# Performance work log

Measured on AMD Instinct MI355X. Metric: run time of the kernel, lower is better.

Reference implementation:

```python
import jax, jax.numpy as jnp
import numpy as np

WS = 7       # window_size
SHIFT = 3    # shift_size
NH = 4       # num_heads


def _layernorm(x, g, b, eps=1e-5):
    m = jnp.mean(x, axis=-1, keepdims=True)
    v = jnp.mean((x - m) ** 2, axis=-1, keepdims=True)
    return (x - m) * jax.lax.rsqrt(v + eps) * g + b


def _mha(x, wq, bq, wk, bk, wv, bv, wo, bo):
    # x: [n, s, c]; weights stored as [in, out]
    n, s, c = x.shape
    dk = c // NH
    q = (x @ wq + bq).reshape(n, s, NH, dk).transpose(0, 2, 1, 3)
    k = (x @ wk + bk).reshape(n, s, NH, dk).transpose(0, 2, 1, 3)
    v = (x @ wv + bv).reshape(n, s, NH, dk).transpose(0, 2, 1, 3)
    scores = jnp.einsum('nhqd,nhkd->nhqk', q, k) / jnp.sqrt(jnp.float32(dk))
    attn = jax.nn.softmax(scores, axis=-1)  # dropout is identity in eval
    out = jnp.einsum('nhqk,nhkd->nhqd', attn, v)
    out = out.transpose(0, 2, 1, 3).reshape(n, s, c)
    return out @ wo + bo


def _window_partition(x):
    B, H, W, C = x.shape
    x = x.reshape(B, H // WS, WS, W // WS, WS, C)
    x = x.transpose(0, 1, 3, 2, 4, 5)
    return x.reshape(-1, WS * WS, C)


def _window_reverse(wins, H, W):
    C = wins.shape[-1]
    B = wins.shape[0] // ((H // WS) * (W // WS))
    x = wins.reshape(B, H // WS, W // WS, WS, WS, C)
    x = x.transpose(0, 1, 3, 2, 4, 5)
    return x.reshape(B, H, W, C)


def setup_inputs() -> dict:
    key = jax.random.key(0)
    ks = jax.random.split(key, 16)
    C = 128
    def w(k, shape):
        return jax.random.normal(k, shape, dtype=jnp.float32) * 0.02
    return {
        'x':  jax.random.normal(ks[0], (4, 56, 56, C), dtype=jnp.float32),
        'wq': w(ks[1], (C, C)), 'bq': jnp.zeros((C,), jnp.float32),
        'wk': w(ks[2], (C, C)), 'bk': jnp.zeros((C,), jnp.float32),
        'wv': w(ks[3], (C, C)), 'bv': jnp.zeros((C,), jnp.float32),
        'wo': w(ks[4], (C, C)), 'bo': jnp.zeros((C,), jnp.float32),
        'w1': w(ks[5], (C, 4 * C)), 'b1': jnp.zeros((4 * C,), jnp.float32),
        'w2': w(ks[6], (4 * C, C)), 'b2': jnp.zeros((C,), jnp.float32),
        'g1': jnp.ones((C,), jnp.float32), 'be1': jnp.zeros((C,), jnp.float32),
        'g2': jnp.ones((C,), jnp.float32), 'be2': jnp.zeros((C,), jnp.float32),
    }


def reference(x, wq, bq, wk, bk, wv, bv, wo, bo, w1, b1, w2, b2, g1, be1, g2, be2):
    B, H, W, C = x.shape
    # cyclic shift
    xs = jnp.roll(x, shift=(-SHIFT, -SHIFT), axis=(1, 2)) if SHIFT > 0 else x
    # windowed attention (note: original code replaces x, no residual here)
    wins = _window_partition(xs)                         # [B*nW, 49, C]
    attn_wins = _mha(wins, wq, bq, wk, bk, wv, bv, wo, bo)
    xs = _window_reverse(attn_wins, H, W)
    x = jnp.roll(xs, shift=(SHIFT, SHIFT), axis=(1, 2)) if SHIFT > 0 else xs
    # global attention residual branch (flatten H*W tokens)
    xf = x.reshape(B, H * W, C)
    xf = xf + _mha(_layernorm(xf, g1, be1), wq, bq, wk, bk, wv, bv, wo, bo)
    # MLP residual branch
    h = jax.nn.gelu(_layernorm(xf, g2, be2) @ w1 + b1, approximate=False)
    xf = xf + (h @ w2 + b2)
    return xf.reshape(B, H, W, C)
```

## Files before the change

kernel.cpp:

```cpp
#include <hip/hip_runtime.h>
#include <hip/hip_bf16.h>
#include <math.h>

#define NH 4
#define DK 32
#define CC 128
#define HW 56
#define SHIFT 3
#define NTOK 12544
#define S_GLB 3136
#define VTW_STRIDE 12608
#define SCALE_L2E 0.25503488f

typedef unsigned short u16;
typedef short bf16x8 __attribute__((ext_vector_type(8)));
typedef unsigned short u16x8 __attribute__((ext_vector_type(8)));
typedef float f32x4 __attribute__((ext_vector_type(4)));

static __device__ __forceinline__ u16 f2bf(float f) {
  unsigned int b = __builtin_bit_cast(unsigned int, f);
  return (u16)((b + 0x7FFFu + ((b >> 16) & 1u)) >> 16);
}
static __device__ __forceinline__ unsigned pk2bf(float a, float b) {
  unsigned r;
  asm("v_cvt_pk_bf16_f32 %0, %1, %2" : "=v"(r) : "v"(a), "v"(b));
  return r;
}
static __device__ __forceinline__ float fexp2(float x) {
  float r;
  asm("v_exp_f32 %0, %1" : "=v"(r) : "v"(x));
  return r;
}

__global__ __launch_bounds__(256) void cvt_all_k(
    const float* __restrict__ w1, const float* __restrict__ w2,
    const float* __restrict__ wq, const float* __restrict__ wk,
    const float* __restrict__ wv, const float* __restrict__ wo,
    u16* __restrict__ w1t, u16* __restrict__ w2t,
    u16* __restrict__ wqkvt, u16* __restrict__ wot) {
  const int idx = blockIdx.x * 256 + threadIdx.x;
  if (idx < 65536) {
    const int c = idx >> 7, r = idx & 127;
    w1t[idx] = f2bf(w1[r * 512 + c]);
  } else if (idx < 131072) {
    const int o = idx - 65536;
    const int c = o / 512, r = o - c * 512;
    w2t[o] = f2bf(w2[r * 128 + c]);
  } else {
    const int o = idx - 131072;
    const int which = o >> 14, oo = o & 16383;
    const int c = oo >> 7, r = oo & 127;
    const float* src = (which == 0) ? wq : (which == 1) ? wk : (which == 2) ? wv : wo;
    u16* dst = (which < 3) ? (wqkvt + which * 16384) : wot;
    dst[oo] = f2bf(src[r * 128 + c]);
  }
}

__global__ __launch_bounds__(256) void win_gather_k(
    const float* __restrict__ x, u16* __restrict__ xg) {
  const int t = blockIdx.x * 2 + (threadIdx.x >> 7);
  const int c = threadIdx.x & 127;
  const int win = t / 49, tok = t % 49;
  const int b = win >> 6, wrem = win & 63;
  const int wi = wrem >> 3, wj = wrem & 7;
  const int i = tok / 7, j = tok % 7;
  int hh = wi * 7 + i + SHIFT; if (hh >= HW) hh -= HW;
  int ww = wj * 7 + j + SHIFT; if (ww >= HW) ww -= HW;
  xg[(size_t)t * CC + c] = f2bf(x[((size_t)(b * HW + hh) * HW + ww) * CC + c]);
}

template <int PATH>
__global__ __launch_bounds__(256) void qkv_gemm_k(
    const u16* __restrict__ xin, const u16* __restrict__ wqkvt,
    const float* __restrict__ bq, const float* __restrict__ bk,
    const float* __restrict__ bv,
    u16* __restrict__ qo, u16* __restrict__ ko, u16* __restrict__ vto) {
  __shared__ __align__(16) u16 xs[64][136];
  __shared__ __align__(16) u16 wt[64][136];
  const int tid = threadIdx.x;
  const int w = tid >> 6, lane = tid & 63;
  const int lo = lane & 15, hi = lane >> 4, hi4 = hi * 4;
  const int m0 = blockIdx.x * 64;
  const int widx = blockIdx.y >> 1;
  const int n0 = (blockIdx.y & 1) * 64;
  {
    const int r = tid >> 2, sg = tid & 3;
    const u16* sx = &xin[(size_t)(m0 + r) * CC + sg * 32];
    const u16* sw = &wqkvt[(size_t)widx * CC * CC + (size_t)(n0 + r) * CC + sg * 32];
#pragma unroll
    for (int j = 0; j < 4; ++j) {
      *reinterpret_cast<u16x8*>(&xs[r][sg * 32 + j * 8]) = *reinterpret_cast<const u16x8*>(&sx[j * 8]);
      *reinterpret_cast<u16x8*>(&wt[r][sg * 32 + j * 8]) = *reinterpret_cast<const u16x8*>(&sw[j * 8]);
    }
  }
  __syncthreads();
  if (widx < 2) {
    const float* bias = (widx == 0) ? bq : bk;
    u16* outp = (widx == 0) ? qo : ko;
    const float oscale = (widx == 0) ? SCALE_L2E : 1.0f;
    f32x4 acc[4];
#pragma unroll
    for (int st = 0; st < 4; ++st) {
      const float b_ = bias[n0 + st * 16 + lo];
      acc[st] = (f32x4){b_, b_, b_, b_};
    }
#pragma unroll
    for (int kk = 0; kk < 4; ++kk) {
      const bf16x8 af = *reinterpret_cast<const bf16x8*>(&xs[w * 16 + lo][kk * 32 + 8 * hi]);
#pragma unroll
      for (int st = 0; st < 4; ++st) {
        const bf16x8 bfr = *reinterpret_cast<const bf16x8*>(&wt[st * 16 + lo][kk * 32 + 8 * hi]);
        acc[st] = __builtin_amdgcn_mfma_f32_16x16x32_bf16(af, bfr, acc[st], 0, 0, 0);
      }
    }
#pragma unroll
    for (int r = 0; r < 4; ++r) {
      const int mm = m0 + w * 16 + hi4 + r;
      size_t rowbase, hstride;
      if (PATH == 0) {
        const int win = mm / 49, tok = mm - win * 49;
        rowbase = ((size_t)(win * 4) * 49 + tok) * DK;
        hstride = (size_t)49 * DK;
      } else {
        const int b = mm / S_GLB, s = mm - b * S_GLB;
        rowbase = ((size_t)(b * 4) * S_GLB + s) * DK;
        hstride = (size_t)S_GLB * DK;
      }
#pragma unroll
      for (int st = 0; st < 4; ++st) {
        const int c = n0 + st * 16 + lo, h = c >> 5, d = c & 31;
        outp[rowbase + (size_t)h * hstride + d] = f2bf(acc[st][r] * oscale);
      }
    }
  } else {
    f32x4 bias4;
#pragma unroll
    for (int r = 0; r < 4; ++r) bias4[r] = bv[n0 + w * 16 + hi4 + r];
    f32x4 acc[4];
#pragma unroll
    for (int st = 0; st < 4; ++st) acc[st] = bias4;
#pragma unroll
    for (int kk = 0; kk < 4; ++kk) {
      const bf16x8 af = *reinterpret_cast<const bf16x8*>(&wt[w * 16 + lo][kk * 32 + 8 * hi]);
#pragma unroll
      for (int st = 0; st < 4; ++st) {
        const bf16x8 bfr = *reinterpret_cast<const bf16x8*>(&xs[st * 16 + lo][kk * 32 + 8 * hi]);
        acc[st] = __builtin_amdgcn_mfma_f32_16x16x32_bf16(af, bfr, acc[st], 0, 0, 0);
      }
    }
#pragma unroll
    for (int st = 0; st < 4; ++st) {
      const int mm = m0 + st * 16 + lo;
#pragma unroll
      for (int r = 0; r < 4; ++r) {
        const int c = n0 + w * 16 + hi4 + r;
        if (PATH == 0) {
          vto[(size_t)c * VTW_STRIDE + mm] = f2bf(acc[st][r]);
        } else {
          const int b = mm / S_GLB, s = mm - b * S_GLB;
          vto[((size_t)b * CC + c) * S_GLB + s] = f2bf(acc[st][r]);
        }
      }
    }
  }
}

__global__ __launch_bounds__(256) void win_attn_k(
    const u16* __restrict__ qw, const u16* __restrict__ kw,
    const u16* __restrict__ vtw, u16* __restrict__ aow) {
  __shared__ __align__(16) u16 psh[4][16][72];
  const int tid = threadIdx.x;
  const int wvi = tid >> 6, lane = tid & 63;
  const int lo = lane & 15, hi = lane >> 4, hi4 = hi * 4;
  const int wh = blockIdx.x * 4 + wvi;
  const int win = wh >> 2, hd = wh & 3;
  const f32x4 zero4 = {0.f, 0.f, 0.f, 0.f};
  bf16x8 ones;
#pragma unroll
  for (int j = 0; j < 8; ++j) ones[j] = (short)0x3F80;

  bf16x8 kf[4], vf[2][2];
#pragma unroll
  for (int st = 0; st < 4; ++st)
    kf[st] = *reinterpret_cast<const bf16x8*>(&kw[((size_t)wh * 49 + st * 16 + lo) * DK + 8 * hi]);
#pragma unroll
  for (int dst = 0; dst < 2; ++dst)
#pragma unroll
    for (int kch = 0; kch < 2; ++kch)
      vf[dst][kch] = *reinterpret_cast<const bf16x8*>(
          &vtw[(size_t)(hd * DK + dst * 16 + lo) * VTW_STRIDE + win * 49 + kch * 32 + 8 * hi]);

#pragma unroll
  for (int g = 0; g < 4; ++g) {
    const bf16x8 qf = *reinterpret_cast<const bf16x8*>(
        &qw[((size_t)wh * 49 + g * 16 + lo) * DK + 8 * hi]);
    f32x4 s4[4];
#pragma unroll
    for (int st = 0; st < 4; ++st) {
      s4[st] = __builtin_amdgcn_mfma_f32_16x16x32_bf16(kf[st], qf, zero4, 0, 0, 0);
#pragma unroll
      for (int r = 0; r < 4; ++r)
        if (st * 16 + hi4 + r >= 49) s4[st][r] = -1e30f;
    }
#pragma unroll
    for (int st = 0; st < 4; ++st) {
      uint2 pk;
      pk.x = pk2bf(fexp2(s4[st][0]), fexp2(s4[st][1]));
      pk.y = pk2bf(fexp2(s4[st][2]), fexp2(s4[st][3]));
      *reinterpret_cast<uint2*>(&psh[wvi][lo][st * 16 + hi4]) = pk;
    }
    asm volatile("" ::: "memory");
    f32x4 acc0 = zero4, acc1 = zero4, lacc = zero4;
#pragma unroll
    for (int kch = 0; kch < 2; ++kch) {
      const bf16x8 pa = *reinterpret_cast<const bf16x8*>(&psh[wvi][lo][kch * 32 + 8 * hi]);
      acc0 = __builtin_amdgcn_mfma_f32_16x16x32_bf16(pa, vf[0][kch], acc0, 0, 0, 0);
      acc1 = __builtin_amdgcn_mfma_f32_16x16x32_bf16(pa, vf[1][kch], acc1, 0, 0, 0);
      lacc = __builtin_amdgcn_mfma_f32_16x16x32_bf16(pa, ones, lacc, 0, 0, 0);
    }
#pragma unroll
    for (int r = 0; r < 4; ++r) {
      const int qrow = g * 16 + hi4 + r;
      if (qrow < 49) {
        const float rl = 1.0f / lacc[r];
        const size_t tw = (size_t)win * 49 + qrow;
        aow[tw * CC + hd * DK + lo] = f2bf(acc0[r] * rl);
        aow[tw * CC + hd * DK + 16 + lo] = f2bf(acc1[r] * rl);
      }
    }
  }
}

__global__ __launch_bounds__(256) void glb_attn_k(
    const u16* __restrict__ qg, const u16* __restrict__ kg,
    const u16* __restrict__ vtg, u16* __restrict__ aog) {
  __shared__ __align__(16) u16 ksh[2][64][40];
  __shared__ __align__(16) u16 vtsh[2][32][72];
  __shared__ __align__(16) u16 psh[4][16][72];
  const int tid = threadIdx.x;
  const int w = tid >> 6, lane = tid & 63;
  const int lo = lane & 15, hi = lane >> 4, hi4 = hi * 4;
  const int bh = blockIdx.y;
  const int q0 = blockIdx.x * 64;
  const f32x4 zero4 = {0.f, 0.f, 0.f, 0.f};
  bf16x8 ones;
#pragma unroll
  for (int j = 0; j < 8; ++j) ones[j] = (short)0x3F80;

  const bf16x8 qfrag = *reinterpret_cast<const bf16x8*>(
      &qg[((size_t)bh * S_GLB + q0 + w * 16 + lo) * DK + 8 * hi]);
  const u16* kg0 = kg + (size_t)bh * S_GLB * DK;
  const u16* vg0 = vtg + (size_t)bh * DK * S_GLB;

  f32x4 oacc0 = zero4, oacc1 = zero4, lacc = zero4;

  const int krow = tid >> 2, kc = tid & 3;
  const int vrow = tid >> 3, vc = tid & 7;

  *reinterpret_cast<u16x8*>(&ksh[0][krow][kc * 8]) =
      *reinterpret_cast<const u16x8*>(&kg0[(size_t)krow * DK + kc * 8]);
  *reinterpret_cast<u16x8*>(&vtsh[0][vrow][vc * 8]) =
      *reinterpret_cast<const u16x8*>(&vg0[(size_t)vrow * S_GLB + vc * 8]);
  __syncthreads();

  for (int kt = 0; kt < 49; ++kt) {
    const int cur = kt & 1, nxt = cur ^ 1;
    u16x8 knext, vnext;
    const bool have = (kt + 1) < 49;
    if (have) {
      knext = *reinterpret_cast<const u16x8*>(
          &kg0[(size_t)((kt + 1) * 64 + krow) * DK + kc * 8]);
      vnext = *reinterpret_cast<const u16x8*>(
          &vg0[(size_t)vrow * S_GLB + (kt + 1) * 64 + vc * 8]);
    }
    f32x4 s4[4];
#pragma unroll
    for (int st = 0; st < 4; ++st) {
      const bf16x8 kfrag = *reinterpret_cast<const bf16x8*>(&ksh[cur][st * 16 + lo][8 * hi]);
      s4[st] = __builtin_amdgcn_mfma_f32_16x16x32_bf16(kfrag, qfrag, zero4, 0, 0, 0);
    }
#pragma unroll
    for (int st = 0; st < 4; ++st) {
      uint2 pk;
      pk.x = pk2bf(fexp2(s4[st][0]), fexp2(s4[st][1]));
      pk.y = pk2bf(fexp2(s4[st][2]), fexp2(s4[st][3]));
      *reinterpret_cast<uint2*>(&psh[w][lo][st * 16 + hi4]) = pk;
    }
    asm volatile("" ::: "memory");
#pragma unroll
    for (int kch = 0; kch < 2; ++kch) {
      const bf16x8 pa = *reinterpret_cast<const bf16x8*>(&psh[w][lo][kch * 32 + 8 * hi]);
      const bf16x8 v0 = *reinterpret_cast<const bf16x8*>(&vtsh[cur][lo][kch * 32 + 8 * hi]);
      const bf16x8 v1 = *reinterpret_cast<const bf16x8*>(&vtsh[cur][16 + lo][kch * 32 + 8 * hi]);
      oacc0 = __builtin_amdgcn_mfma_f32_16x16x32_bf16(pa, v0, oacc0, 0, 0, 0);
      oacc1 = __builtin_amdgcn_mfma_f32_16x16x32_bf16(pa, v1, oacc1, 0, 0, 0);
      lacc = __builtin_amdgcn_mfma_f32_16x16x32_bf16(pa, ones, lacc, 0, 0, 0);
    }
    if (have) {
      *reinterpret_cast<u16x8*>(&ksh[nxt][krow][kc * 8]) = knext;
      *reinterpret_cast<u16x8*>(&vtsh[nxt][vrow][vc * 8]) = vnext;
    }
    __syncthreads();
  }

  const int b = bh >> 2, hd = bh & 3;
#pragma unroll
  for (int r = 0; r < 4; ++r) {
    const float rl = 1.0f / lacc[r];
    const size_t t = (size_t)b * S_GLB + q0 + w * 16 + hi4 + r;
    aog[t * CC + hd * DK + lo] = f2bf(oacc0[r] * rl);
    aog[t * CC + hd * DK + 16 + lo] = f2bf(oacc1[r] * rl);
  }
}

template <int MODE>
__global__ __launch_bounds__(256) void proj_gemm_k(
    const u16* __restrict__ ain, const u16* __restrict__ wot,
    const float* __restrict__ bo, const float* __restrict__ resid,
    float* __restrict__ xfo) {
  __shared__ __align__(16) u16 xs[64][136];
  __shared__ __align__(16) u16 wt[64][136];
  const int tid = threadIdx.x;
  const int w = tid >> 6, lane = tid & 63;
  const int lo = lane & 15, hi = lane >> 4, hi4 = hi * 4;
  const int m0 = blockIdx.x * 64;
  const int n0 = blockIdx.y * 64;
  {
    const int r = tid >> 2, sg = tid & 3;
    const u16* sx = &ain[(size_t)(m0 + r) * CC + sg * 32];
    const u16* sw = &wot[(size_t)(n0 + r) * CC + sg * 32];
#pragma unroll
    for (int j = 0; j < 4; ++j) {
      *reinterpret_cast<u16x8*>(&xs[r][sg * 32 + j * 8]) = *reinterpret_cast<const u16x8*>(&sx[j * 8]);
      *reinterpret_cast<u16x8*>(&wt[r][sg * 32 + j * 8]) = *reinterpret_cast<const u16x8*>(&sw[j * 8]);
    }
  }
  __syncthreads();
  f32x4 acc[4];
#pragma unroll
  for (int st = 0; st < 4; ++st) {
    const float b_ = bo[n0 + st * 16 + lo];
    acc[st] = (f32x4){b_, b_, b_, b_};
  }
#pragma unroll
  for (int kk = 0; kk < 4; ++kk) {
    const bf16x8 af = *reinterpret_cast<const bf16x8*>(&xs[w * 16 + lo][kk * 32 + 8 * hi]);
#pragma unroll
    for (int st = 0; st < 4; ++st) {
      const bf16x8 bfr = *reinterpret_cast<const bf16x8*>(&wt[st * 16 + lo][kk * 32 + 8 * hi]);
      acc[st] = __builtin_amdgcn_mfma_f32_16x16x32_bf16(af, bfr, acc[st], 0, 0, 0);
    }
  }
#pragma unroll
  for (int r = 0; r < 4; ++r) {
    const int mm = m0 + w * 16 + hi4 + r;
    size_t trow;
    if (MODE == 0) {
      const int win = mm / 49, tok = mm - win * 49;
      const int b = win >> 6, wi = (win >> 3) & 7, wj = win & 7;
      const int ii = tok / 7, jj = tok - ii * 7;
      int hr = wi * 7 + ii + SHIFT; if (hr >= HW) hr -= HW;
      int wr = wj * 7 + jj + SHIFT; if (wr >= HW) wr -= HW;
      trow = ((size_t)b * S_GLB + hr * HW + wr) * CC;
    } else {
      trow = (size_t)mm * CC;
    }
#pragma unroll
    for (int st = 0; st < 4; ++st) {
      const int c = n0 + st * 16 + lo;
      if (MODE == 1)
        xfo[trow + c] = resid[trow + c] + acc[st][r];
      else
        xfo[trow + c] = acc[st][r];
    }
  }
}

__global__ __launch_bounds__(128) void ln_k(
    const float* __restrict__ xf, const float* __restrict__ g,
    const float* __restrict__ be, u16* __restrict__ ybf) {
  __shared__ float xs[8][CC];
  __shared__ float red[8][2];
  const int t0 = blockIdx.x * 8;
  const int tid = threadIdx.x;
  for (int t2 = 0; t2 < 8; ++t2) xs[t2][tid] = xf[(size_t)(t0 + t2) * CC + tid];
  __syncthreads();
  const int wvi = tid >> 6, lane = tid & 63;
  for (int t2 = wvi * 4; t2 < wvi * 4 + 4; ++t2) {
    const float v0 = xs[t2][lane], v1 = xs[t2][64 + lane];
    float s = v0 + v1, sq = v0 * v0 + v1 * v1;
#pragma unroll
    for (int off = 1; off < 64; off <<= 1) { s += __shfl_xor(s, off); sq += __shfl_xor(sq, off); }
    if (lane == 0) {
      const float mu = s * 0.0078125f;
      const float var = sq * 0.0078125f - mu * mu;
      red[t2][0] = mu; red[t2][1] = rsqrtf(var + 1e-5f);
    }
  }
  __syncthreads();
  const float gg = g[tid], bb = be[tid];
  for (int t2 = 0; t2 < 8; ++t2)
    ybf[(size_t)(t0 + t2) * CC + tid] = f2bf((xs[t2][tid] - red[t2][0]) * red[t2][1] * gg + bb);
}

__global__ __launch_bounds__(256) void gemm1_k(
    const u16* __restrict__ ybf, const u16* __restrict__ w1t,
    const float* __restrict__ b1, u16* __restrict__ hb) {
  __shared__ __align__(16) u16 xs[64][136];
  __shared__ __align__(16) u16 wt[64][136];
  const int tid = threadIdx.x;
  const int w = tid >> 6, lane = tid & 63;
  const int lo = lane & 15, hi = lane >> 4;
  const int m0 = blockIdx.x * 64, n0 = blockIdx.y * 64;
  {
    const int r = tid >> 2, sg = tid & 3;
    const u16* src_x = &ybf[(size_t)(m0 + r) * CC + sg * 32];
    const u16* src_w = &w1t[(size_t)(n0 + r) * CC + sg * 32];
#pragma unroll
    for (int j = 0; j < 4; ++j) {
      *reinterpret_cast<u16x8*>(&xs[r][sg * 32 + j * 8]) = *reinterpret_cast<const u16x8*>(&src_x[j * 8]);
      *reinterpret_cast<u16x8*>(&wt[r][sg * 32 + j * 8]) = *reinterpret_cast<const u16x8*>(&src_w[j * 8]);
    }
  }
  __syncthreads();
  f32x4 acc[4];
#pragma unroll
  for (int st = 0; st < 4; ++st) {
    const float bv = b1[n0 + st * 16 + lo];
    acc[st] = (f32x4){bv, bv, bv, bv};
  }
#pragma unroll
  for (int kk = 0; kk < 4; ++kk) {
    const bf16x8 af = *reinterpret_cast<const bf16x8*>(&xs[w * 16 + lo][kk * 32 + 8 * hi]);
#pragma unroll
    for (int st = 0; st < 4; ++st) {
      const bf16x8 bfr = *reinterpret_cast<const bf16x8*>(&wt[st * 16 + lo][kk * 32 + 8 * hi]);
      acc[st] = __builtin_amdgcn_mfma_f32_16x16x32_bf16(af, bfr, acc[st], 0, 0, 0);
    }
  }
#pragma unroll
  for (int st = 0; st < 4; ++st) {
#pragma unroll
    for (int r = 0; r < 4; ++r) {
      const float val = acc[st][r];
      const float gel = 0.5f * val * (1.0f + erff(val * 0.70710678118f));
      hb[(size_t)(m0 + w * 16 + (hi << 2) + r) * 512 + n0 + st * 16 + lo] = f2bf(gel);
    }
  }
}

__global__ __launch_bounds__(256) void gemm2_k(
    const u16* __restrict__ hb, const u16* __restrict__ w2t,
    const float* __restrict__ b2, const float* __restrict__ xf,
    float* __restrict__ out) {
  __shared__ __align__(16) u16 xs[64][136];
  __shared__ __align__(16) u16 wt[64][136];
  const int tid = threadIdx.x;
  const int w = tid >> 6, lane = tid & 63;
  const int lo = lane & 15, hi = lane >> 4;
  const int m0 = blockIdx.x * 64, n0 = blockIdx.y * 64;
  f32x4 acc[4];
#pragma unroll
  for (int st = 0; st < 4; ++st) {
    const float bv = b2[n0 + st * 16 + lo];
    acc[st] = (f32x4){bv, bv, bv, bv};
  }
  for (int kc = 0; kc < 4; ++kc) {
    if (kc) __syncthreads();
    {
      const int r = tid >> 2, sg = tid & 3;
      const u16* src_x = &hb[(size_t)(m0 + r) * 512 + kc * 128 + sg * 32];
      const u16* src_w = &w2t[(size_t)(n0 + r) * 512 + kc * 128 + sg * 32];
#pragma unroll
      for (int j = 0; j < 4; ++j) {
        *reinterpret_cast<u16x8*>(&xs[r][sg * 32 + j * 8]) = *reinterpret_cast<const u16x8*>(&src_x[j * 8]);
        *reinterpret_cast<u16x8*>(&wt[r][sg * 32 + j * 8]) = *reinterpret_cast<const u16x8*>(&src_w[j * 8]);
      }
    }
    __syncthreads();
#pragma unroll
    for (int kk = 0; kk < 4; ++kk) {
      const bf16x8 af = *reinterpret_cast<const bf16x8*>(&xs[w * 16 + lo][kk * 32 + 8 * hi]);
#pragma unroll
      for (int st = 0; st < 4; ++st) {
        const bf16x8 bfr = *reinterpret_cast<const bf16x8*>(&wt[st * 16 + lo][kk * 32 + 8 * hi]);
        acc[st] = __builtin_amdgcn_mfma_f32_16x16x32_bf16(af, bfr, acc[st], 0, 0, 0);
      }
    }
  }
#pragma unroll
  for (int st = 0; st < 4; ++st) {
#pragma unroll
    for (int r = 0; r < 4; ++r) {
      const size_t idx = (size_t)(m0 + w * 16 + (hi << 2) + r) * CC + n0 + st * 16 + lo;
      out[idx] = xf[idx] + acc[st][r];
    }
  }
}

extern "C" void kernel_launch(void* const* d_in, const int* in_sizes, int n_in,
                              void* d_out, int out_size, void* d_ws, size_t ws_size,
                              hipStream_t stream) {
  (void)in_sizes; (void)n_in; (void)out_size; (void)ws_size;
  const float* x   = (const float*)d_in[0];
  const float* wq  = (const float*)d_in[1];
  const float* bq  = (const float*)d_in[2];
  const float* wk  = (const float*)d_in[3];
  const float* bk  = (const float*)d_in[4];
  const float* wv  = (const float*)d_in[5];
  const float* bv  = (const float*)d_in[6];
  const float* wo  = (const float*)d_in[7];
  const float* bo  = (const float*)d_in[8];
  const float* w1  = (const float*)d_in[9];
  const float* b1  = (const float*)d_in[10];
  const float* w2  = (const float*)d_in[11];
  const float* b2  = (const float*)d_in[12];
  const float* g1  = (const float*)d_in[13];
  const float* be1 = (const float*)d_in[14];
  const float* g2  = (const float*)d_in[15];
  const float* be2 = (const float*)d_in[16];
  float* out = (float*)d_out;

  char* p = (char*)d_ws;
  auto alloc = [&](size_t bytes) { char* r = p; p += (bytes + 255) & ~(size_t)255; return r; };
  float* xf  = (float*)alloc((size_t)NTOK * CC * 4);
  u16* xg    = (u16*)alloc((size_t)NTOK * CC * 2);
  u16* qw    = (u16*)alloc((size_t)NTOK * CC * 2 + 4096);
  u16* kw    = (u16*)alloc((size_t)NTOK * CC * 2 + 4096);
  u16* vtw   = (u16*)alloc((size_t)CC * VTW_STRIDE * 2);
  u16* aow   = (u16*)alloc((size_t)NTOK * CC * 2);
  u16* hb    = (u16*)alloc((size_t)NTOK * 512 * 2);
  u16* wqkvt = (u16*)alloc(3 * 16384 * 2);
  u16* wot   = (u16*)alloc(16384 * 2);
  u16* w1t   = (u16*)alloc(65536 * 2);
  u16* w2t   = (u16*)alloc(65536 * 2);

  cvt_all_k<<<768, 256, 0, stream>>>(w1, w2, wq, wk, wv, wo, w1t, w2t, wqkvt, wot);

  win_gather_k<<<NTOK / 2, 256, 0, stream>>>(x, xg);
  qkv_gemm_k<0><<<dim3(NTOK / 64, 6), 256, 0, stream>>>(xg, wqkvt, bq, bk, bv, qw, kw, vtw);
  win_attn_k<<<256, 256, 0, stream>>>(qw, kw, vtw, aow);
  proj_gemm_k<0><<<dim3(NTOK / 64, 2), 256, 0, stream>>>(aow, wot, bo, nullptr, xf);

  ln_k<<<NTOK / 8, 128, 0, stream>>>(xf, g1, be1, xg);
  qkv_gemm_k<1><<<dim3(NTOK / 64, 6), 256, 0, stream>>>(xg, wqkvt, bq, bk, bv, qw, kw, vtw);
  glb_attn_k<<<dim3(S_GLB / 64, 16), 256, 0, stream>>>(qw, kw, vtw, aow);
  proj_gemm_k<1><<<dim3(NTOK / 64, 2), 256, 0, stream>>>(aow, wot, bo, xf, xf);

  ln_k<<<NTOK / 8, 128, 0, stream>>>(xf, g2, be2, xg);
  gemm1_k<<<dim3(NTOK / 64, 8), 256, 0, stream>>>(xg, w1t, b1, hb);
  gemm2_k<<<dim3(NTOK / 64, 2), 256, 0, stream>>>(hb, w2t, b2, xf, out);
}
```

Before: 135.0 us.

## Fuse LayerNorm into GEMM prologues and use direct-to-LDS loads in global attention

Removes the standalone LayerNorm kernels by computing row mean/variance and normalization inside the QKV and MLP-up GEMM tile loads from fp32 input. The global attention kernel switches to global_load_lds asynchronous copies into unpadded shared buffers with an XOR swizzle on P and V^T to avoid bank conflicts. This removes two launches and intermediate bf16 traffic but recomputes LayerNorm redundantly for every N-tile block and reads fp32 rather than bf16.

```diff
diff --git a/kernel.cpp b/kernel.cpp
--- a/kernel.cpp
+++ b/kernel.cpp
@@ -30,6 +30,11 @@
   float r;
   asm("v_exp_f32 %0, %1" : "=v"(r) : "v"(x));
   return r;
+}
+static __device__ __forceinline__ void gload16(const void* g, void* l) {
+  __builtin_amdgcn_global_load_lds(
+      (const __attribute__((address_space(1))) unsigned int*)g,
+      (__attribute__((address_space(3))) unsigned int*)l, 16, 0, 0);
 }
 
 __global__ __launch_bounds__(256) void cvt_all_k(
@@ -71,7 +76,9 @@
 
 template <int PATH>
 __global__ __launch_bounds__(256) void qkv_gemm_k(
-    const u16* __restrict__ xin, const u16* __restrict__ wqkvt,
+    const u16* __restrict__ xin, const float* __restrict__ xfin,
+    const float* __restrict__ lng, const float* __restrict__ lnb,
+    const u16* __restrict__ wqkvt,
     const float* __restrict__ bq, const float* __restrict__ bk,
     const float* __restrict__ bv,
     u16* __restrict__ qo, u16* __restrict__ ko, u16* __restrict__ vto) {
@@ -85,13 +92,38 @@
   const int n0 = (blockIdx.y & 1) * 64;
   {
     const int r = tid >> 2, sg = tid & 3;
-    const u16* sx = &xin[(size_t)(m0 + r) * CC + sg * 32];
+    if (PATH == 0) {
+      const u16* sx = &xin[(size_t)(m0 + r) * CC + sg * 32];
+#pragma unroll
+      for (int j = 0; j < 4; ++j)
+        *reinterpret_cast<u16x8*>(&xs[r][sg * 32 + j * 8]) = *reinterpret_cast<const u16x8*>(&sx[j * 8]);
+    } else {
+      const float* sx = &xfin[(size_t)(m0 + r) * CC + sg * 32];
+      float vb[32];
+      float s = 0.f, sq = 0.f;
+#pragma unroll
+      for (int j = 0; j < 32; j += 4) {
+        const float4 f = *reinterpret_cast<const float4*>(&sx[j]);
+        vb[j] = f.x; vb[j + 1] = f.y; vb[j + 2] = f.z; vb[j + 3] = f.w;
+        s += (f.x + f.y) + (f.z + f.w);
+        sq += (f.x * f.x + f.y * f.y) + (f.z * f.z + f.w * f.w);
+      }
+      s += __shfl_xor(s, 1);  s += __shfl_xor(s, 2);
+      sq += __shfl_xor(sq, 1); sq += __shfl_xor(sq, 2);
+      const float mu = s * 0.0078125f;
+      const float rsig = rsqrtf(sq * 0.0078125f - mu * mu + 1e-5f);
+#pragma unroll
+      for (int j = 0; j < 32; j += 2) {
+        const int c = sg * 32 + j;
+        const float a = (vb[j] - mu) * rsig * lng[c] + lnb[c];
+        const float b_ = (vb[j + 1] - mu) * rsig * lng[c + 1] + lnb[c + 1];
+        *reinterpret_cast<unsigned*>(&xs[r][c]) = pk2bf(a, b_);
+      }
+    }
     const u16* sw = &wqkvt[(size_t)widx * CC * CC + (size_t)(n0 + r) * CC + sg * 32];
 #pragma unroll
-    for (int j = 0; j < 4; ++j) {
-      *reinterpret_cast<u16x8*>(&xs[r][sg * 32 + j * 8]) = *reinterpret_cast<const u16x8*>(&sx[j * 8]);
+    for (int j = 0; j < 4; ++j)
       *reinterpret_cast<u16x8*>(&wt[r][sg * 32 + j * 8]) = *reinterpret_cast<const u16x8*>(&sw[j * 8]);
-    }
   }
   __syncthreads();
   if (widx < 2) {
@@ -234,9 +266,9 @@
 __global__ __launch_bounds__(256) void glb_attn_k(
     const u16* __restrict__ qg, const u16* __restrict__ kg,
     const u16* __restrict__ vtg, u16* __restrict__ aog) {
-  __shared__ __align__(16) u16 ksh[2][64][40];
-  __shared__ __align__(16) u16 vtsh[2][32][72];
-  __shared__ __align__(16) u16 psh[4][16][72];
+  __shared__ __align__(16) u16 ksh[2][64][32];
+  __shared__ __align__(16) u16 vtsh[2][32][64];
+  __shared__ __align__(16) u16 psh[4][16][64];
   const int tid = threadIdx.x;
   const int w = tid >> 6, lane = tid & 63;
   const int lo = lane & 15, hi = lane >> 4, hi4 = hi * 4;
@@ -252,26 +284,26 @@
   const u16* kg0 = kg + (size_t)bh * S_GLB * DK;
   const u16* vg0 = vtg + (size_t)bh * DK * S_GLB;
 
+  const u16* ksrc = kg0 + (size_t)(w * 16 + (lane >> 2)) * DK + (lane & 3) * 8;
+  const u16* vsrc = vg0 + (size_t)(w * 8 + (lane >> 3)) * S_GLB + ((lane & 7) ^ (lane >> 3)) * 8;
+  u16* kdst0 = &ksh[0][w * 16][0]; u16* kdst1 = &ksh[1][w * 16][0];
+  u16* vdst0 = &vtsh[0][w * 8][0]; u16* vdst1 = &vtsh[1][w * 8][0];
+
   f32x4 oacc0 = zero4, oacc1 = zero4, lacc = zero4;
 
-  const int krow = tid >> 2, kc = tid & 3;
-  const int vrow = tid >> 3, vc = tid & 7;
-
-  *reinterpret_cast<u16x8*>(&ksh[0][krow][kc * 8]) =
-      *reinterpret_cast<const u16x8*>(&kg0[(size_t)krow * DK + kc * 8]);
-  *reinterpret_cast<u16x8*>(&vtsh[0][vrow][vc * 8]) =
-      *reinterpret_cast<const u16x8*>(&vg0[(size_t)vrow * S_GLB + vc * 8]);
+  gload16(ksrc, kdst0);
+  gload16(vsrc, vdst0);
   __syncthreads();
 
+  char* const pbase = (char*)&psh[w][lo][0];
+  char* const vbase0 = (char*)&vtsh[0][0][0];
+  const unsigned swz = (unsigned)(lo & 7) << 4;
+
   for (int kt = 0; kt < 49; ++kt) {
-    const int cur = kt & 1, nxt = cur ^ 1;
-    u16x8 knext, vnext;
-    const bool have = (kt + 1) < 49;
-    if (have) {
-      knext = *reinterpret_cast<const u16x8*>(
-          &kg0[(size_t)((kt + 1) * 64 + krow) * DK + kc * 8]);
-      vnext = *reinterpret_cast<const u16x8*>(
-          &vg0[(size_t)vrow * S_GLB + (kt + 1) * 64 + vc * 8]);
+    const int cur = kt & 1;
+    if (kt + 1 < 49) {
+      gload16(ksrc + (size_t)(kt + 1) * 64 * DK, cur ? kdst0 : kdst1);
+      gload16(vsrc + (size_t)(kt + 1) * 64, cur ? vdst0 : vdst1);
     }
     f32x4 s4[4];
 #pragma unroll
@@ -284,21 +316,19 @@
       uint2 pk;
       pk.x = pk2bf(fexp2(s4[st][0]), fexp2(s4[st][1]));
       pk.y = pk2bf(fexp2(s4[st][2]), fexp2(s4[st][3]));
-      *reinterpret_cast<uint2*>(&psh[w][lo][st * 16 + hi4]) = pk;
+      *reinterpret_cast<uint2*>(pbase + (((unsigned)(st * 32 + hi * 8)) ^ swz)) = pk;
     }
     asm volatile("" ::: "memory");
+    char* const vrow0 = vbase0 + (size_t)cur * (32 * 64 * 2) + lo * 128;
 #pragma unroll
     for (int kch = 0; kch < 2; ++kch) {
-      const bf16x8 pa = *reinterpret_cast<const bf16x8*>(&psh[w][lo][kch * 32 + 8 * hi]);
-      const bf16x8 v0 = *reinterpret_cast<const bf16x8*>(&vtsh[cur][lo][kch * 32 + 8 * hi]);
-      const bf16x8 v1 = *reinterpret_cast<const bf16x8*>(&vtsh[cur][16 + lo][kch * 32 + 8 * hi]);
+      const unsigned off = ((unsigned)(kch * 64 + hi * 16)) ^ swz;
+      const bf16x8 pa = *reinterpret_cast<const bf16x8*>(pbase + off);
+      const bf16x8 v0 = *reinterpret_cast<const bf16x8*>(vrow0 + off);
+      const bf16x8 v1 = *reinterpret_cast<const bf16x8*>(vrow0 + 16 * 128 + off);
       oacc0 = __builtin_amdgcn_mfma_f32_16x16x32_bf16(pa, v0, oacc0, 0, 0, 0);
       oacc1 = __builtin_amdgcn_mfma_f32_16x16x32_bf16(pa, v1, oacc1, 0, 0, 0);
       lacc = __builtin_amdgcn_mfma_f32_16x16x32_bf16(pa, ones, lacc, 0, 0, 0);
-    }
-    if (have) {
-      *reinterpret_cast<u16x8*>(&ksh[nxt][krow][kc * 8]) = knext;
-      *reinterpret_cast<u16x8*>(&vtsh[nxt][vrow][vc * 8]) = vnext;
     }
     __syncthreads();
   }
@@ -376,35 +406,9 @@
   }
 }
 
-__global__ __launch_bounds__(128) void ln_k(
-    const float* __restrict__ xf, const float* __restrict__ g,
-    const float* __restrict__ be, u16* __restrict__ ybf) {
-  __shared__ float xs[8][CC];
-  __shared__ float red[8][2];
-  const int t0 = blockIdx.x * 8;
-  const int tid = threadIdx.x;
-  for (int t2 = 0; t2 < 8; ++t2) xs[t2][tid] = xf[(size_t)(t0 + t2) * CC + tid];
-  __syncthreads();
-  const int wvi = tid >> 6, lane = tid & 63;
-  for (int t2 = wvi * 4; t2 < wvi * 4 + 4; ++t2) {
-    const float v0 = xs[t2][lane], v1 = xs[t2][64 + lane];
-    float s = v0 + v1, sq = v0 * v0 + v1 * v1;
-#pragma unroll
-    for (int off = 1; off < 64; off <<= 1) { s += __shfl_xor(s, off); sq += __shfl_xor(sq, off); }
-    if (lane == 0) {
-      const float mu = s * 0.0078125f;
-      const float var = sq * 0.0078125f - mu * mu;
-      red[t2][0] = mu; red[t2][1] = rsqrtf(var + 1e-5f);
-    }
-  }
-  __syncthreads();
-  const float gg = g[tid], bb = be[tid];
-  for (int t2 = 0; t2 < 8; ++t2)
-    ybf[(size_t)(t0 + t2) * CC + tid] = f2bf((xs[t2][tid] - red[t2][0]) * red[t2][1] * gg + bb);
-}
-
 __global__ __launch_bounds__(256) void gemm1_k(
-    const u16* __restrict__ ybf, const u16* __restrict__ w1t,
+    const float* __restrict__ xfin, const float* __restrict__ lng,
+    const float* __restrict__ lnb, const u16* __restrict__ w1t,
     const float* __restrict__ b1, u16* __restrict__ hb) {
   __shared__ __align__(16) u16 xs[64][136];
   __shared__ __align__(16) u16 wt[64][136];
@@ -414,13 +418,31 @@
   const int m0 = blockIdx.x * 64, n0 = blockIdx.y * 64;
   {
     const int r = tid >> 2, sg = tid & 3;
-    const u16* src_x = &ybf[(size_t)(m0 + r) * CC + sg * 32];
+    const float* sx = &xfin[(size_t)(m0 + r) * CC + sg * 32];
+    float vb[32];
+    float s = 0.f, sq = 0.f;
+#pragma unroll
+    for (int j = 0; j < 32; j += 4) {
+      const float4 f = *reinterpret_cast<const float4*>(&sx[j]);
+      vb[j] = f.x; vb[j + 1] = f.y; vb[j + 2] = f.z; vb[j + 3] = f.w;
+      s += (f.x + f.y) + (f.z + f.w);
+      sq += (f.x * f.x + f.y * f.y) + (f.z * f.z + f.w * f.w);
+    }
+    s += __shfl_xor(s, 1);  s += __shfl_xor(s, 2);
+    sq += __shfl_xor(sq, 1); sq += __shfl_xor(sq, 2);
+    const float mu = s * 0.0078125f;
+    const float rsig = rsqrtf(sq * 0.0078125f - mu * mu + 1e-5f);
+#pragma unroll
+    for (int j = 0; j < 32; j += 2) {
+      const int c = sg * 32 + j;
+      const float a = (vb[j] - mu) * rsig * lng[c] + lnb[c];
+      const float b_ = (vb[j + 1] - mu) * rsig * lng[c + 1] + lnb[c + 1];
+      *reinterpret_cast<unsigned*>(&xs[r][c]) = pk2bf(a, b_);
+    }
     const u16* src_w = &w1t[(size_t)(n0 + r) * CC + sg * 32];
 #pragma unroll
-    for (int j = 0; j < 4; ++j) {
-      *reinterpret_cast<u16x8*>(&xs[r][sg * 32 + j * 8]) = *reinterpret_cast<const u16x8*>(&src_x[j * 8]);
+    for (int j = 0; j < 4; ++j)
       *reinterpret_cast<u16x8*>(&wt[r][sg * 32 + j * 8]) = *reinterpret_cast<const u16x8*>(&src_w[j * 8]);
-    }
   }
   __syncthreads();
   f32x4 acc[4];
@@ -538,16 +560,16 @@
   cvt_all_k<<<768, 256, 0, stream>>>(w1, w2, wq, wk, wv, wo, w1t, w2t, wqkvt, wot);
 
   win_gather_k<<<NTOK / 2, 256, 0, stream>>>(x, xg);
-  qkv_gemm_k<0><<<dim3(NTOK / 64, 6), 256, 0, stream>>>(xg, wqkvt, bq, bk, bv, qw, kw, vtw);
+  qkv_gemm_k<0><<<dim3(NTOK / 64, 6), 256, 0, stream>>>(
+      xg, nullptr, nullptr, nullptr, wqkvt, bq, bk, bv, qw, kw, vtw);
   win_attn_k<<<256, 256, 0, stream>>>(qw, kw, vtw, aow);
   proj_gemm_k<0><<<dim3(NTOK / 64, 2), 256, 0, stream>>>(aow, wot, bo, nullptr, xf);
 
-  ln_k<<<NTOK / 8, 128, 0, stream>>>(xf, g1, be1, xg);
-  qkv_gemm_k<1><<<dim3(NTOK / 64, 6), 256, 0, stream>>>(xg, wqkvt, bq, bk, bv, qw, kw, vtw);
+  qkv_gemm_k<1><<<dim3(NTOK / 64, 6), 256, 0, stream>>>(
+      nullptr, xf, g1, be1, wqkvt, bq, bk, bv, qw, kw, vtw);
   glb_attn_k<<<dim3(S_GLB / 64, 16), 256, 0, stream>>>(qw, kw, vtw, aow);
   proj_gemm_k<1><<<dim3(NTOK / 64, 2), 256, 0, stream>>>(aow, wot, bo, xf, xf);
 
-  ln_k<<<NTOK / 8, 128, 0, stream>>>(xf, g2, be2, xg);
-  gemm1_k<<<dim3(NTOK / 64, 8), 256, 0, stream>>>(xg, w1t, b1, hb);
+  gemm1_k<<<dim3(NTOK / 64, 8), 256, 0, stream>>>(xf, g2, be2, w1t, b1, hb);
   gemm2_k<<<dim3(NTOK / 64, 2), 256, 0, stream>>>(hb, w2t, b2, xf, out);
 }
```

Result: slower. 139.6 us (+3.4%).

## Split global attention over two key halves and combine partials in a separate kernel

Applied to the files above, without the earlier changes.

The global attention kernel now splits the 49 key tiles into two halves along a third grid dimension, doubling the number of blocks so more of the GPU is occupied. Each half writes unnormalized fp32 partial outputs and row sums, and a new combine kernel adds the two and normalizes into bf16. K/V staging now uses direct global-to-LDS loads with unpadded, XOR-swizzled shared layouts in place of register round-trips and padding. The cost is an extra kernel launch plus several MB of fp32 partial traffic written and read back.

```diff
diff --git a/kernel.cpp b/kernel.cpp
--- a/kernel.cpp
+++ b/kernel.cpp
@@ -30,6 +30,11 @@
   float r;
   asm("v_exp_f32 %0, %1" : "=v"(r) : "v"(x));
   return r;
+}
+static __device__ __forceinline__ void gload16(const void* g, void* l) {
+  __builtin_amdgcn_global_load_lds(
+      (const __attribute__((address_space(1))) unsigned int*)g,
+      (__attribute__((address_space(3))) unsigned int*)l, 16, 0, 0);
 }
 
 __global__ __launch_bounds__(256) void cvt_all_k(
@@ -69,6 +74,33 @@
   xg[(size_t)t * CC + c] = f2bf(x[((size_t)(b * HW + hh) * HW + ww) * CC + c]);
 }
 
+__global__ __launch_bounds__(128) void ln_k(
+    const float* __restrict__ xf, const float* __restrict__ g,
+    const float* __restrict__ be, u16* __restrict__ ybf) {
+  __shared__ float xs[8][CC];
+  __shared__ float red[8][2];
+  const int t0 = blockIdx.x * 8;
+  const int tid = threadIdx.x;
+  for (int t2 = 0; t2 < 8; ++t2) xs[t2][tid] = xf[(size_t)(t0 + t2) * CC + tid];
+  __syncthreads();
+  const int wvi = tid >> 6, lane = tid & 63;
+  for (int t2 = wvi * 4; t2 < wvi * 4 + 4; ++t2) {
+    const float v0 = xs[t2][lane], v1 = xs[t2][64 + lane];
+    float s = v0 + v1, sq = v0 * v0 + v1 * v1;
+#pragma unroll
+    for (int off = 1; off < 64; off <<= 1) { s += __shfl_xor(s, off); sq += __shfl_xor(sq, off); }
+    if (lane == 0) {
+      const float mu = s * 0.0078125f;
+      const float var = sq * 0.0078125f - mu * mu;
+      red[t2][0] = mu; red[t2][1] = rsqrtf(var + 1e-5f);
+    }
+  }
+  __syncthreads();
+  const float gg = g[tid], bb = be[tid];
+  for (int t2 = 0; t2 < 8; ++t2)
+    ybf[(size_t)(t0 + t2) * CC + tid] = f2bf((xs[t2][tid] - red[t2][0]) * red[t2][1] * gg + bb);
+}
+
 template <int PATH>
 __global__ __launch_bounds__(256) void qkv_gemm_k(
     const u16* __restrict__ xin, const u16* __restrict__ wqkvt,
@@ -233,15 +265,18 @@
 
 __global__ __launch_bounds__(256) void glb_attn_k(
     const u16* __restrict__ qg, const u16* __restrict__ kg,
-    const u16* __restrict__ vtg, u16* __restrict__ aog) {
-  __shared__ __align__(16) u16 ksh[2][64][40];
-  __shared__ __align__(16) u16 vtsh[2][32][72];
-  __shared__ __align__(16) u16 psh[4][16][72];
+    const u16* __restrict__ vtg, float* __restrict__ po, float* __restrict__ pl) {
+  __shared__ __align__(16) u16 ksh[2][64][32];
+  __shared__ __align__(16) u16 vtsh[2][32][64];
+  __shared__ __align__(16) u16 psh[4][16][64];
   const int tid = threadIdx.x;
   const int w = tid >> 6, lane = tid & 63;
   const int lo = lane & 15, hi = lane >> 4, hi4 = hi * 4;
   const int bh = blockIdx.y;
   const int q0 = blockIdx.x * 64;
+  const int sp = blockIdx.z;
+  const int kt_beg = sp * 25;
+  const int kt_end = sp ? 49 : 25;
   const f32x4 zero4 = {0.f, 0.f, 0.f, 0.f};
   bf16x8 ones;
 #pragma unroll
@@ -252,26 +287,26 @@
   const u16* kg0 = kg + (size_t)bh * S_GLB * DK;
   const u16* vg0 = vtg + (size_t)bh * DK * S_GLB;
 
+  const u16* ksrc = kg0 + (size_t)(w * 16 + (lane >> 2)) * DK + (lane & 3) * 8;
+  const u16* vsrc = vg0 + (size_t)(w * 8 + (lane >> 3)) * S_GLB + ((lane & 7) ^ (lane >> 3)) * 8;
+  u16* kdst0 = &ksh[0][w * 16][0]; u16* kdst1 = &ksh[1][w * 16][0];
+  u16* vdst0 = &vtsh[0][w * 8][0]; u16* vdst1 = &vtsh[1][w * 8][0];
+
   f32x4 oacc0 = zero4, oacc1 = zero4, lacc = zero4;
 
-  const int krow = tid >> 2, kc = tid & 3;
-  const int vrow = tid >> 3, vc = tid & 7;
-
-  *reinterpret_cast<u16x8*>(&ksh[0][krow][kc * 8]) =
-      *reinterpret_cast<const u16x8*>(&kg0[(size_t)krow * DK + kc * 8]);
-  *reinterpret_cast<u16x8*>(&vtsh[0][vrow][vc * 8]) =
-      *reinterpret_cast<const u16x8*>(&vg0[(size_t)vrow * S_GLB + vc * 8]);
+  gload16(ksrc + (size_t)kt_beg * 64 * DK, kdst0);
+  gload16(vsrc + (size_t)kt_beg * 64, vdst0);
   __syncthreads();
 
-  for (int kt = 0; kt < 49; ++kt) {
-    const int cur = kt & 1, nxt = cur ^ 1;
-    u16x8 knext, vnext;
-    const bool have = (kt + 1) < 49;
-    if (have) {
-      knext = *reinterpret_cast<const u16x8*>(
-          &kg0[(size_t)((kt + 1) * 64 + krow) * DK + kc * 8]);
-      vnext = *reinterpret_cast<const u16x8*>(
-          &vg0[(size_t)vrow * S_GLB + (kt + 1) * 64 + vc * 8]);
+  char* const pbase = (char*)&psh[w][lo][0];
+  char* const vbase0 = (char*)&vtsh[0][0][0];
+  const unsigned swz = (unsigned)(lo & 7) << 4;
+
+  for (int kt = kt_beg; kt < kt_end; ++kt) {
+    const int cur = (kt - kt_beg) & 1;
+    if (kt + 1 < kt_end) {
+      gload16(ksrc + (size_t)(kt + 1) * 64 * DK, cur ? kdst0 : kdst1);
+      gload16(vsrc + (size_t)(kt + 1) * 64, cur ? vdst0 : vdst1);
     }
     f32x4 s4[4];
 #pragma unroll
@@ -284,33 +319,45 @@
       uint2 pk;
       pk.x = pk2bf(fexp2(s4[st][0]), fexp2(s4[st][1]));
       pk.y = pk2bf(fexp2(s4[st][2]), fexp2(s4[st][3]));
-      *reinterpret_cast<uint2*>(&psh[w][lo][st * 16 + hi4]) = pk;
+      *reinterpret_cast<uint2*>(pbase + (((unsigned)(st * 32 + hi * 8)) ^ swz)) = pk;
     }
     asm volatile("" ::: "memory");
+    char* const vrow0 = vbase0 + (size_t)cur * (32 * 64 * 2) + lo * 128;
 #pragma unroll
     for (int kch = 0; kch < 2; ++kch) {
-      const bf16x8 pa = *reinterpret_cast<const bf16x8*>(&psh[w][lo][kch * 32 + 8 * hi]);
-      const bf16x8 v0 = *reinterpret_cast<const bf16x8*>(&vtsh[cur][lo][kch * 32 + 8 * hi]);
-      const bf16x8 v1 = *reinterpret_cast<const bf16x8*>(&vtsh[cur][16 + lo][kch * 32 + 8 * hi]);
+      const unsigned off = ((unsigned)(kch * 64 + hi * 16)) ^ swz;
+      const bf16x8 pa = *reinterpret_cast<const bf16x8*>(pbase + off);
+      const bf16x8 v0 = *reinterpret_cast<const bf16x8*>(vrow0 + off);
+      const bf16x8 v1 = *reinterpret_cast<const bf16x8*>(vrow0 + 16 * 128 + off);
       oacc0 = __builtin_amdgcn_mfma_f32_16x16x32_bf16(pa, v0, oacc0, 0, 0, 0);
       oacc1 = __builtin_amdgcn_mfma_f32_16x16x32_bf16(pa, v1, oacc1, 0, 0, 0);
       lacc = __builtin_amdgcn_mfma_f32_16x16x32_bf16(pa, ones, lacc, 0, 0, 0);
     }
-    if (have) {
-      *reinterpret_cast<u16x8*>(&ksh[nxt][krow][kc * 8]) = knext;
-      *reinterpret_cast<u16x8*>(&vtsh[nxt][vrow][vc * 8]) = vnext;
-    }
     __syncthreads();
   }
 
   const int b = bh >> 2, hd = bh & 3;
+  float* pob = po + (size_t)sp * NTOK * CC;
 #pragma unroll
   for (int r = 0; r < 4; ++r) {
-    const float rl = 1.0f / lacc[r];
     const size_t t = (size_t)b * S_GLB + q0 + w * 16 + hi4 + r;
-    aog[t * CC + hd * DK + lo] = f2bf(oacc0[r] * rl);
-    aog[t * CC + hd * DK + 16 + lo] = f2bf(oacc1[r] * rl);
-  }
+    pob[t * CC + hd * DK + lo] = oacc0[r];
+    pob[t * CC + hd * DK + 16 + lo] = oacc1[r];
+    if (lo == 0)
+      pl[((size_t)sp * 16 + bh) * S_GLB + q0 + w * 16 + hi4 + r] = lacc[r];
+  }
+}
+
+__global__ __launch_bounds__(256) void combine_k(
+    const float* __restrict__ po, const float* __restrict__ pl,
+    u16* __restrict__ aog) {
+  const int t = blockIdx.x * 2 + (threadIdx.x >> 7);
+  const int c = threadIdx.x & 127;
+  const int b = t / S_GLB, s = t - b * S_GLB;
+  const int bh = b * 4 + (c >> 5);
+  const float l = pl[(size_t)bh * S_GLB + s] + pl[((size_t)16 + bh) * S_GLB + s];
+  const float v = po[(size_t)t * CC + c] + po[(size_t)NTOK * CC + (size_t)t * CC + c];
+  aog[(size_t)t * CC + c] = f2bf(v / l);
 }
 
 template <int MODE>
@@ -374,33 +421,6 @@
         xfo[trow + c] = acc[st][r];
     }
   }
-}
-
-__global__ __launch_bounds__(128) void ln_k(
-    const float* __restrict__ xf, const float* __restrict__ g,
-    const float* __restrict__ be, u16* __restrict__ ybf) {
-  __shared__ float xs[8][CC];
-  __shared__ float red[8][2];
-  const int t0 = blockIdx.x * 8;
-  const int tid = threadIdx.x;
-  for (int t2 = 0; t2 < 8; ++t2) xs[t2][tid] = xf[(size_t)(t0 + t2) * CC + tid];
-  __syncthreads();
-  const int wvi = tid >> 6, lane = tid & 63;
-  for (int t2 = wvi * 4; t2 < wvi * 4 + 4; ++t2) {
-    const float v0 = xs[t2][lane], v1 = xs[t2][64 + lane];
-    float s = v0 + v1, sq = v0 * v0 + v1 * v1;
-#pragma unroll
-    for (int off = 1; off < 64; off <<= 1) { s += __shfl_xor(s, off); sq += __shfl_xor(sq, off); }
-    if (lane == 0) {
-      const float mu = s * 0.0078125f;
-      const float var = sq * 0.0078125f - mu * mu;
-      red[t2][0] = mu; red[t2][1] = rsqrtf(var + 1e-5f);
-    }
-  }
-  __syncthreads();
-  const float gg = g[tid], bb = be[tid];
-  for (int t2 = 0; t2 < 8; ++t2)
-    ybf[(size_t)(t0 + t2) * CC + tid] = f2bf((xs[t2][tid] - red[t2][0]) * red[t2][1] * gg + bb);
 }
 
 __global__ __launch_bounds__(256) void gemm1_k(
@@ -530,6 +550,8 @@
   u16* vtw   = (u16*)alloc((size_t)CC * VTW_STRIDE * 2);
   u16* aow   = (u16*)alloc((size_t)NTOK * CC * 2);
   u16* hb    = (u16*)alloc((size_t)NTOK * 512 * 2);
+  float* po  = (float*)alloc((size_t)2 * NTOK * CC * 4);
+  float* pl  = (float*)alloc((size_t)2 * 16 * S_GLB * 4);
   u16* wqkvt = (u16*)alloc(3 * 16384 * 2);
   u16* wot   = (u16*)alloc(16384 * 2);
   u16* w1t   = (u16*)alloc(65536 * 2);
@@ -544,7 +566,8 @@
 
   ln_k<<<NTOK / 8, 128, 0, stream>>>(xf, g1, be1, xg);
   qkv_gemm_k<1><<<dim3(NTOK / 64, 6), 256, 0, stream>>>(xg, wqkvt, bq, bk, bv, qw, kw, vtw);
-  glb_attn_k<<<dim3(S_GLB / 64, 16), 256, 0, stream>>>(qw, kw, vtw, aow);
+  glb_attn_k<<<dim3(S_GLB / 64, 16, 2), 256, 0, stream>>>(qw, kw, vtw, po, pl);
+  combine_k<<<NTOK / 2, 256, 0, stream>>>(po, pl, aow);
   proj_gemm_k<1><<<dim3(NTOK / 64, 2), 256, 0, stream>>>(aow, wot, bo, xf, xf);
 
   ln_k<<<NTOK / 8, 128, 0, stream>>>(xf, g2, be2, xg);
```

Result: faster. 123.3 us (-8.7%).
